# Kernel tuning notes

Hardware: AMD Instinct MI355X
Metric: run time of the kernel (lower is better)

Reference implementation:

```python
import jax, jax.numpy as jnp
import numpy as np

N, E, MUL, NATTR, NBASIS, HID = 50000, 800000, 32, 16, 8, 8
AVG_NEIGH = 16.0


def setup_inputs() -> dict:
    key = jax.random.key(0)
    ks = jax.random.split(key, 13)
    return {
        "x": jax.random.normal(ks[0], (N, NATTR), jnp.float32),
        "h": jax.random.normal(ks[1], (N, 4 * MUL), jnp.float32),
        "edge_length_embeddings": jax.random.uniform(ks[2], (E, NBASIS), jnp.float32),
        "edge_sh": jax.random.normal(ks[3], (E, 4), jnp.float32),
        "edge_index": jax.random.randint(ks[4], (2, E), 0, N),
        "W1_s": jax.random.normal(ks[5], (MUL, MUL), jnp.float32),
        "W1_v": jax.random.normal(ks[6], (MUL, MUL), jnp.float32),
        "fc_w1": jax.random.normal(ks[7], (NBASIS, HID), jnp.float32),
        "fc_w2": jax.random.normal(ks[8], (HID, 4 * MUL), jnp.float32),
        "Wsc_s": jax.random.normal(ks[9], (MUL, NATTR, MUL), jnp.float32),
        "Wsc_v": jax.random.normal(ks[10], (MUL, NATTR, MUL), jnp.float32),
        "W2_s": jax.random.normal(ks[11], (2 * MUL, MUL), jnp.float32),
        "W2_v": jax.random.normal(ks[12], (2 * MUL, MUL), jnp.float32),
    }


def reference(x, h, edge_length_embeddings, edge_sh, edge_index,
              W1_s, W1_v, fc_w1, fc_w2, Wsc_s, Wsc_v, W2_s, W2_v):
    # h layout: [N, 32 scalars (0e) | 32 vectors (1o) flattened]
    h_s0 = h[:, :MUL]                      # [N, 32]
    h_v0 = h[:, MUL:].reshape(-1, MUL, 3)  # [N, 32, 3]

    # self-connection: FullyConnectedTensorProduct(feat, node_attr 16x0e -> feat)
    inv_sc = float(1.0 / np.sqrt(MUL * NATTR))
    sc_s = jnp.einsum('nu,nv,uvw->nw', h_s0, x, Wsc_s) * inv_sc    # [N, 32]
    sc_v = jnp.einsum('num,nv,uvw->nwm', h_v0, x, Wsc_v) * inv_sc  # [N, 32, 3]

    # linear_1 (per-irrep linear, fan-in normalized)
    inv_m = float(1.0 / np.sqrt(MUL))
    h_s = (h_s0 @ W1_s) * inv_m
    h_v = jnp.einsum('num,uw->nwm', h_v0, W1_v) * inv_m

    # radial MLP: [8] -> silu -> [8] -> [tp.weight_numel = 4*32]
    z = jax.nn.silu((edge_length_embeddings @ fc_w1) * float(1.0 / np.sqrt(NBASIS)))
    w = (z @ fc_w2) * float(1.0 / np.sqrt(HID))        # [E, 128]
    wA, wB, wC, wD = jnp.split(w, 4, axis=1)           # each [E, 32]

    src = edge_index[1]
    dst = edge_index[0]
    hs_e = h_s[src]   # [E, 32]  gather
    hv_e = h_v[src]   # [E, 32, 3]
    sh0 = edge_sh[:, 0:1]   # [E, 1]
    sh1 = edge_sh[:, 1:4]   # [E, 3]

    # 4 'uvu' CG paths (edge mul = 1), per-edge weights from radial MLP
    sA = hs_e * sh0 * wA                                            # 0e x 0e -> 0e
    sD = jnp.einsum('eum,em->eu', hv_e, sh1) * wD * float(1.0 / np.sqrt(3.0))  # 1o x 1o -> 0e
    vB = hs_e[:, :, None] * sh1[:, None, :] * wB[:, :, None]        # 0e x 1o -> 1o
    vC = hv_e * sh0[:, :, None] * wC[:, :, None]                    # 1o x 0e -> 1o

    mid_s = jnp.concatenate([sA, sD], axis=1)   # [E, 64]  (sorted irreps_mid, 0e block)
    mid_v = jnp.concatenate([vB, vC], axis=1)   # [E, 64, 3] (1o block)

    # scatter-sum over destination nodes
    agg_s = jax.ops.segment_sum(mid_s, dst, num_segments=N)
    agg_v = jax.ops.segment_sum(mid_v, dst, num_segments=N)
    inv_n = float(1.0 / np.sqrt(AVG_NEIGH))
    agg_s = agg_s * inv_n
    agg_v = agg_v * inv_n

    # linear_2: 64x0e+64x1o -> 32x0e+32x1o
    inv2 = float(1.0 / np.sqrt(2 * MUL))
    out_s = (agg_s @ W2_s) * inv2 + sc_s
    out_v = jnp.einsum('num,uw->nwm', agg_v, W2_v) * inv2 + sc_v

    return jnp.concatenate([out_s, out_v.reshape(-1, 3 * MUL)], axis=1)  # [N, 128]
```

## Files before the change

### kernel.cpp

```cpp
#include <hip/hip_runtime.h>
#include <hip/hip_bf16.h>

#define NN 50000
#define EE 800000
#define SCAN_B 196

typedef unsigned short u16;
typedef unsigned int u32;
typedef float f32x16 __attribute__((ext_vector_type(16)));
typedef short bf16x8_t __attribute__((ext_vector_type(8)));

__device__ __forceinline__ float bfu2f(u16 b) { return __builtin_bit_cast(float, ((u32)b) << 16); }
__device__ __forceinline__ float lo16(u32 d) { return __builtin_bit_cast(float, d << 16); }
__device__ __forceinline__ float hi16(u32 d) { return __builtin_bit_cast(float, d & 0xffff0000u); }
__device__ __forceinline__ u16 f2bfu(float f) {
    u32 u = __builtin_bit_cast(u32, f);
    u32 r = (u + 0x7fffu + ((u >> 16) & 1u)) >> 16;
    return (u16)r;
}
__device__ __forceinline__ u32 cvt_pk_bf16(float lo, float hi) {
    u32 r;
    asm("v_cvt_pk_bf16_f32 %0, %1, %2" : "=v"(r) : "v"(lo), "v"(hi));
    return r;
}

__global__ __launch_bounds__(256) void k_hist(const int* __restrict__ eidx, int* __restrict__ deg) {
    int e = blockIdx.x * 256 + threadIdx.x;
    atomicAdd(&deg[eidx[e]], 1);
}

__global__ __launch_bounds__(256) void k_scan1(const int* __restrict__ deg, int* __restrict__ bsum) {
    __shared__ int red[256];
    const int tid = threadIdx.x;
    int i = blockIdx.x * 256 + tid;
    int v = (i < NN) ? deg[i] : 0;
    red[tid] = v;
    __syncthreads();
    for (int off = 128; off > 0; off >>= 1) {
        if (tid < off) red[tid] += red[tid + off];
        __syncthreads();
    }
    if (tid == 0) bsum[blockIdx.x] = red[0];
}

__global__ __launch_bounds__(256) void k_scan2(
    const int* __restrict__ deg, const int* __restrict__ bsum, int* __restrict__ row_ptr,
    const float* __restrict__ Wscs, const float* __restrict__ Wscv,
    const float* __restrict__ W1s, const float* __restrict__ W1v,
    u16* __restrict__ wscsT, u16* __restrict__ wscvT,
    u16* __restrict__ w1sT, u16* __restrict__ w1vT)
{
    const int b = blockIdx.x;
    const int tid = threadIdx.x;
    if (b >= SCAN_B) {
        int i = (b - SCAN_B) * 256 + tid;
        if (i < 16384) {
            int u = i >> 9, v = (i >> 5) & 15, w = i & 31;
            wscsT[(u * 32 + w) * 16 + v] = f2bfu(Wscs[i]);
            wscvT[(u * 32 + w) * 16 + v] = f2bfu(Wscv[i]);
        }
        if (i < 1024) {
            int u = i >> 5, w = i & 31;
            w1sT[w * 32 + u] = f2bfu(W1s[i]);
            w1vT[w * 32 + u] = f2bfu(W1v[i]);
        }
        return;
    }
    __shared__ int pre[256];
    __shared__ int bpre;
    int pv = (tid < b) ? bsum[tid] : 0;
    pre[tid] = pv;
    __syncthreads();
    for (int off = 128; off > 0; off >>= 1) {
        if (tid < off) pre[tid] += pre[tid + off];
        __syncthreads();
    }
    if (tid == 0) bpre = pre[0];
    __syncthreads();
    int i = b * 256 + tid;
    int v = (i < NN) ? deg[i] : 0;
    pre[tid] = v;
    __syncthreads();
    for (int off = 1; off < 256; off <<= 1) {
        int t = (tid >= off) ? pre[tid - off] : 0;
        __syncthreads();
        pre[tid] += t;
        __syncthreads();
    }
    int excl = pre[tid] - v;
    if (i <= NN) row_ptr[i] = bpre + excl;
}

__global__ __launch_bounds__(256) void k2a_edge(
    const float* __restrict__ emb, const float* __restrict__ esh,
    const int* __restrict__ eidx, const float* __restrict__ fc1,
    const int* __restrict__ row_ptr, int* __restrict__ cursor,
    u32* __restrict__ edata)
{
    __shared__ float sfc1[64];
    const int tid = threadIdx.x;
    if (tid < 64) sfc1[tid] = fc1[tid];
    __syncthreads();
    int e = blockIdx.x * 256 + tid;
    const float invb = 0.3535533905932738f;
    float4 ea = *(const float4*)(emb + (size_t)e * 8);
    float4 eb = *(const float4*)(emb + (size_t)e * 8 + 4);
    float em[8] = {ea.x, ea.y, ea.z, ea.w, eb.x, eb.y, eb.z, eb.w};
    float z[8];
#pragma unroll
    for (int k = 0; k < 8; k++) {
        float t = 0.f;
#pragma unroll
        for (int j = 0; j < 8; j++) t += em[j] * sfc1[j * 8 + k];
        t *= invb;
        z[k] = (t / (1.f + __expf(-t))) * invb;
    }
    float4 sh = *(const float4*)(esh + (size_t)e * 4);
    int dst = eidx[e], src = eidx[EE + e];
    int p = atomicAdd(&cursor[dst], 1);
    size_t slot = (size_t)row_ptr[dst] + p;
    u32* wp = edata + slot * 8;
    uint4 A, B;
    A.x = cvt_pk_bf16(z[0], z[1]);
    A.y = cvt_pk_bf16(z[2], z[3]);
    A.z = cvt_pk_bf16(z[4], z[5]);
    A.w = cvt_pk_bf16(z[6], z[7]);
    B.x = cvt_pk_bf16(sh.x, sh.y);
    B.y = cvt_pk_bf16(sh.z, sh.w);
    B.z = ((u32)src) << 8;
    B.w = 0;
    *(uint4*)wp = A;
    *(uint4*)(wp + 4) = B;
}

__global__ __launch_bounds__(64) void k1_mfma(
    const float* __restrict__ x, const float* __restrict__ h,
    const u16* __restrict__ wscsT, const u16* __restrict__ wscvT,
    const u16* __restrict__ w1sT, const u16* __restrict__ w1vT,
    u16* __restrict__ hsv, float* __restrict__ out)
{
    __shared__ __align__(16) u16 sh[64 * 32 * 2];
    u32* sh32 = (u32*)sh;
    const int l = threadIdx.x;
    const int base = blockIdx.x * 32;
    const int n = l & 31;
    const int hi = l >> 5;

    {
        int r = base + (l >> 1);
        if (r >= NN) r = NN - 1;
        const float* hp = h + (size_t)r * 128 + (l & 1) * 64;
        int nn = l >> 1;
        int cp0 = (l & 1) * 32;
#pragma unroll
        for (int q = 0; q < 16; q++) {
            float4 f = *(const float4*)(hp + q * 4);
            sh32[(cp0 + 2 * q + 0) * 32 + nn] = cvt_pk_bf16(f.x, f.y);
            sh32[(cp0 + 2 * q + 1) * 32 + nn] = cvt_pk_bf16(f.z, f.w);
        }
    }
    float xv0, xv1, xv2, xv3, xv4, xv5, xv6, xv7;
    {
        int r = base + n;
        if (r >= NN) r = NN - 1;
        const float* xp = x + (size_t)r * 16 + hi * 8;
        float4 a = *(const float4*)xp;
        float4 b = *(const float4*)(xp + 4);
        xv0 = a.x; xv1 = a.y; xv2 = a.z; xv3 = a.w;
        xv4 = b.x; xv5 = b.y; xv6 = b.z; xv7 = b.w;
    }
    __syncthreads();

    f32x16 accS, accX, accY, accZ;
#pragma unroll
    for (int i = 0; i < 16; i++) { accS[i] = 0.f; accX[i] = 0.f; accY[i] = 0.f; accZ[i] = 0.f; }

#define MK_A(A, s)                                                     \
    { union { u32 w[4]; bf16x8_t v; } t_;                              \
      t_.w[0] = cvt_pk_bf16((s) * xv0, (s) * xv1);                     \
      t_.w[1] = cvt_pk_bf16((s) * xv2, (s) * xv3);                     \
      t_.w[2] = cvt_pk_bf16((s) * xv4, (s) * xv5);                     \
      t_.w[3] = cvt_pk_bf16((s) * xv6, (s) * xv7);                     \
      A = t_.v; }

    const size_t boff = (size_t)n * 16 + hi * 8;
    bf16x8_t Bs = *(const bf16x8_t*)(wscsT + boff);
    bf16x8_t Bv = *(const bf16x8_t*)(wscvT + boff);
#pragma unroll 2
    for (int u = 0; u < 32; u++) {
        bf16x8_t BsN, BvN;
        if (u < 31) {
            BsN = *(const bf16x8_t*)(wscsT + (size_t)(u + 1) * 512 + boff);
            BvN = *(const bf16x8_t*)(wscvT + (size_t)(u + 1) * 512 + boff);
        }
        float hsu = bfu2f(sh[(u >> 1) * 64 + n * 2 + (u & 1)]);
        int c = 32 + 3 * u;
        float hx = bfu2f(sh[(c >> 1) * 64 + n * 2 + (c & 1)]);
        float hy = bfu2f(sh[((c + 1) >> 1) * 64 + n * 2 + ((c + 1) & 1)]);
        float hz = bfu2f(sh[((c + 2) >> 1) * 64 + n * 2 + ((c + 2) & 1)]);
        bf16x8_t A;
        MK_A(A, hsu); accS = __builtin_amdgcn_mfma_f32_32x32x16_bf16(A, Bs, accS, 0, 0, 0);
        MK_A(A, hx);  accX = __builtin_amdgcn_mfma_f32_32x32x16_bf16(A, Bv, accX, 0, 0, 0);
        MK_A(A, hy);  accY = __builtin_amdgcn_mfma_f32_32x32x16_bf16(A, Bv, accY, 0, 0, 0);
        MK_A(A, hz);  accZ = __builtin_amdgcn_mfma_f32_32x32x16_bf16(A, Bv, accZ, 0, 0, 0);
        Bs = BsN; Bv = BvN;
    }
#undef MK_A

    const float inv_sc = 0.04419417382415922f;
#pragma unroll
    for (int r = 0; r < 16; r++) {
        int node2 = base + ((r & 3) + 8 * (r >> 2) + 4 * hi);
        if (node2 < NN) {
            float* op = out + (size_t)node2 * 128;
            op[n] = accS[r] * inv_sc;
            op[32 + n * 3 + 0] = accX[r] * inv_sc;
            op[32 + n * 3 + 1] = accY[r] * inv_sc;
            op[32 + n * 3 + 2] = accZ[r] * inv_sc;
        }
    }

    const float inv_m = 0.17677669529663687f;
    {
        f32x16 aw;
#pragma unroll
        for (int i = 0; i < 16; i++) aw[i] = 0.f;
#pragma unroll
        for (int k0 = 0; k0 < 2; k0++) {
            union { u32 w[4]; bf16x8_t v; } A;
#pragma unroll
            for (int q = 0; q < 4; q++)
                A.w[q] = sh32[(8 * k0 + 4 * hi + q) * 32 + n];
            bf16x8_t B = *(const bf16x8_t*)(w1sT + n * 32 + 16 * k0 + 8 * hi);
            aw = __builtin_amdgcn_mfma_f32_32x32x16_bf16(A.v, B, aw, 0, 0, 0);
        }
#pragma unroll
        for (int r = 0; r < 16; r++) {
            int node2 = base + ((r & 3) + 8 * (r >> 2) + 4 * hi);
            if (node2 < NN) hsv[(size_t)node2 * 128 + n] = f2bfu(aw[r] * inv_m);
        }
    }
#pragma unroll
    for (int m = 0; m < 3; m++) {
        f32x16 aw;
#pragma unroll
        for (int i = 0; i < 16; i++) aw[i] = 0.f;
#pragma unroll
        for (int k0 = 0; k0 < 2; k0++) {
            union { u32 w[4]; bf16x8_t v; } A;
#pragma unroll
            for (int j = 0; j < 8; j += 2) {
                int u0 = 16 * k0 + 8 * hi + j;
                int c0 = 32 + 3 * u0 + m, c1 = c0 + 3;
                u16 a = sh[(c0 >> 1) * 64 + n * 2 + (c0 & 1)];
                u16 b = sh[(c1 >> 1) * 64 + n * 2 + (c1 & 1)];
                A.w[j >> 1] = (u32)a | ((u32)b << 16);
            }
            bf16x8_t B = *(const bf16x8_t*)(w1vT + n * 32 + 16 * k0 + 8 * hi);
            aw = __builtin_amdgcn_mfma_f32_32x32x16_bf16(A.v, B, aw, 0, 0, 0);
        }
#pragma unroll
        for (int r = 0; r < 16; r++) {
            int node2 = base + ((r & 3) + 8 * (r >> 2) + 4 * hi);
            if (node2 < NN) hsv[(size_t)node2 * 128 + 32 + m * 32 + n] = f2bfu(aw[r] * inv_m);
        }
    }
}

__device__ __forceinline__ void edge_body(
    const u32* __restrict__ r, const char* __restrict__ hbase,
    const float* fcs, const float* fcv, bool lo, int o1, int o2, int o3,
    float& acc_s, float& av0, float& av1, float& av2)
{
    uint4 A = *(const uint4*)r;
    uint4 B = *(const uint4*)(r + 4);
    float ws_ = lo16(A.x) * fcs[0] + hi16(A.x) * fcs[1] + lo16(A.y) * fcs[2] + hi16(A.y) * fcs[3]
              + lo16(A.z) * fcs[4] + hi16(A.z) * fcs[5] + lo16(A.w) * fcs[6] + hi16(A.w) * fcs[7];
    float wv_ = lo16(A.x) * fcv[0] + hi16(A.x) * fcv[1] + lo16(A.y) * fcv[2] + hi16(A.y) * fcv[3]
              + lo16(A.z) * fcv[4] + hi16(A.z) * fcv[5] + lo16(A.w) * fcv[6] + hi16(A.w) * fcv[7];
    float sh0 = lo16(B.x), sx = hi16(B.x), sy = lo16(B.y), sz = hi16(B.y);
    const u16* hp = (const u16*)(hbase + B.z);
    float g1 = bfu2f(hp[o1]), g2 = bfu2f(hp[o2]), g3 = bfu2f(hp[o3]);
    float c1 = lo ? sh0 : sx;
    float c2 = lo ? 0.f : sy;
    float c3 = lo ? 0.f : sz;
    acc_s += ws_ * (g1 * c1 + g2 * c2 + g3 * c3);
    float tw = wv_ * sh0;
    float t0 = lo ? wv_ * sx : tw;
    float t1 = lo ? wv_ * sy : tw;
    float t2 = lo ? wv_ * sz : tw;
    av0 += g1 * t0; av1 += g2 * t1; av2 += g3 * t2;
}

__global__ __launch_bounds__(256) void k2b_gather(
    const u32* __restrict__ edata, const float* __restrict__ fc2,
    const u16* __restrict__ hsv, const int* __restrict__ row_ptr,
    const float* __restrict__ W2s, const float* __restrict__ W2v,
    float* __restrict__ out)
{
    __shared__ float sred[4][256];
    const int tid = threadIdx.x;
    const int wv = tid >> 6, lane = tid & 63;
    const int n = blockIdx.x * 4 + wv;
    const int beg = __builtin_amdgcn_readfirstlane(row_ptr[n]);
    const int end = __builtin_amdgcn_readfirstlane(row_ptr[n + 1]);

    const float inv3 = 0.5773502691896258f;
    const int u = lane & 31;
    const bool lo = lane < 32;
    const int cs = lo ? lane : (96 + u);
    const int cv = lo ? (32 + u) : (64 + u);
    const int o1 = lo ? u : (32 + u);
    const int o2 = lo ? u : (64 + u);
    const int o3 = lo ? u : (96 + u);
    float fcs[8], fcv[8];
#pragma unroll
    for (int j = 0; j < 8; j++) {
        float sscale = lo ? 1.f : inv3;
        fcs[j] = fc2[j * 128 + cs] * sscale;
        fcv[j] = fc2[j * 128 + cv];
    }
    const char* hbase = (const char*)hsv;

    float as[4] = {0.f, 0.f, 0.f, 0.f};
    float a0[4] = {0.f, 0.f, 0.f, 0.f};
    float a1[4] = {0.f, 0.f, 0.f, 0.f};
    float a2[4] = {0.f, 0.f, 0.f, 0.f};
    int s = beg;
    for (; s + 3 < end; s += 4) {
        edge_body(edata + (size_t)(s + 0) * 8, hbase, fcs, fcv, lo, o1, o2, o3, as[0], a0[0], a1[0], a2[0]);
        edge_body(edata + (size_t)(s + 1) * 8, hbase, fcs, fcv, lo, o1, o2, o3, as[1], a0[1], a1[1], a2[1]);
        edge_body(edata + (size_t)(s + 2) * 8, hbase, fcs, fcv, lo, o1, o2, o3, as[2], a0[2], a1[2], a2[2]);
        edge_body(edata + (size_t)(s + 3) * 8, hbase, fcs, fcv, lo, o1, o2, o3, as[3], a0[3], a1[3], a2[3]);
    }
    for (; s < end; s++)
        edge_body(edata + (size_t)s * 8, hbase, fcs, fcv, lo, o1, o2, o3, as[0], a0[0], a1[0], a2[0]);
    float acc_s = (as[0] + as[1]) + (as[2] + as[3]);
    float av0 = (a0[0] + a0[1]) + (a0[2] + a0[3]);
    float av1 = (a1[0] + a1[1]) + (a1[2] + a1[3]);
    float av2 = (a2[0] + a2[1]) + (a2[2] + a2[3]);

    float* red = sred[wv];
    red[lane] = acc_s;
    red[64 + lane * 3 + 0] = av0;
    red[64 + lane * 3 + 1] = av1;
    red[64 + lane * 3 + 2] = av2;

    const float sc2 = 0.03125f;
    const int w = lane & 31;
    const int b0 = lo ? 0 : 64;
    const int s0 = lo ? 1 : 3;
    const int b1 = lo ? 66 : 65;
    const float* __restrict__ Wp0 = lo ? W2s : W2v;
    float p0 = 0.f, p1 = 0.f;
#pragma unroll 8
    for (int c = 0; c < 64; c++) {
        float r0 = red[b0 + c * s0];
        float r1 = red[b1 + c * 3];
        p0 += r0 * Wp0[c * 32 + w];
        p1 += r1 * W2v[c * 32 + w];
    }
    const size_t o = (size_t)n * 128;
    const int addr0 = lo ? w : (32 + 3 * w);
    const int addr1 = lo ? (32 + 3 * w + 2) : (32 + 3 * w + 1);
    out[o + addr0] += p0 * sc2;
    out[o + addr1] += p1 * sc2;
}

extern "C" void kernel_launch(void* const* d_in, const int* in_sizes, int n_in,
                              void* d_out, int out_size, void* d_ws, size_t ws_size,
                              hipStream_t stream) {
    const float* x    = (const float*)d_in[0];
    const float* h    = (const float*)d_in[1];
    const float* emb  = (const float*)d_in[2];
    const float* esh  = (const float*)d_in[3];
    const int*   eidx = (const int*)d_in[4];
    const float* W1s  = (const float*)d_in[5];
    const float* W1v  = (const float*)d_in[6];
    const float* fc1  = (const float*)d_in[7];
    const float* fc2  = (const float*)d_in[8];
    const float* Wscs = (const float*)d_in[9];
    const float* Wscv = (const float*)d_in[10];
    const float* W2s  = (const float*)d_in[11];
    const float* W2v  = (const float*)d_in[12];
    float* out = (float*)d_out;

    int* deg      = (int*)d_ws;
    int* row_ptr  = deg + NN;
    int* cursor   = row_ptr + (NN + 1);
    int* bsum     = (int*)d_ws + 150004;
    u32* edata    = (u32*)d_ws + 150208;
    u16* hsv      = (u16*)(edata + (size_t)EE * 8);
    u16* wscsT    = hsv + (size_t)NN * 128;
    u16* wscvT    = wscsT + 16384;
    u16* w1sT     = wscvT + 16384;
    u16* w1vT     = w1sT + 1024;

    hipMemsetAsync(d_ws, 0, (size_t)(3 * NN + 1) * 4, stream);
    k_hist<<<3125, 256, 0, stream>>>(eidx, deg);
    k_scan1<<<SCAN_B, 256, 0, stream>>>(deg, bsum);
    k_scan2<<<SCAN_B + 64, 256, 0, stream>>>(deg, bsum, row_ptr,
                                             Wscs, Wscv, W1s, W1v, wscsT, wscvT, w1sT, w1vT);
    k2a_edge<<<3125, 256, 0, stream>>>(emb, esh, eidx, fc1, row_ptr, cursor, edata);
    k1_mfma<<<(NN + 31) / 32, 64, 0, stream>>>(x, h, wscsT, wscvT, w1sT, w1vT, hsv, out);
    k2b_gather<<<NN / 4, 256, 0, stream>>>(edata, fc2, hsv, row_ptr, W2s, W2v, out);
}
```

Measured before the change: 238.3 us.

## Interleave hsv node layout and fuse node/edge prep kernels

Stores each node's transformed features interleaved per channel (scalar plus three vector components side by side). The gather kernel can then fetch all four values a lane needs with one 8-byte load instead of three scattered 2-byte loads. Two kernel pairs are merged to cut launches and let independent work overlap: weight conversion now runs inside the histogram kernel, and the per-edge radial/CSR fill shares one launch with the per-node MFMA tiles, four waves per block. In exchange, lanes in the low half of each wave load bytes they do not use, and the combined kernel carries extra shared memory per block.

```diff
diff --git a/kernel.cpp b/kernel.cpp
--- a/kernel.cpp
+++ b/kernel.cpp
@@ -24,9 +24,30 @@
     return r;
 }
 
-__global__ __launch_bounds__(256) void k_hist(const int* __restrict__ eidx, int* __restrict__ deg) {
-    int e = blockIdx.x * 256 + threadIdx.x;
-    atomicAdd(&deg[eidx[e]], 1);
+__global__ __launch_bounds__(256) void k_prep(
+    const int* __restrict__ eidx, int* __restrict__ deg,
+    const float* __restrict__ Wscs, const float* __restrict__ Wscv,
+    const float* __restrict__ W1s, const float* __restrict__ W1v,
+    u16* __restrict__ wscsT, u16* __restrict__ wscvT,
+    u16* __restrict__ w1sT, u16* __restrict__ w1vT)
+{
+    const int b = blockIdx.x;
+    if (b < 3125) {
+        int e = b * 256 + threadIdx.x;
+        atomicAdd(&deg[eidx[e]], 1);
+    } else {
+        int i = (b - 3125) * 256 + threadIdx.x;
+        if (i < 16384) {
+            int u = i >> 9, v = (i >> 5) & 15, w = i & 31;
+            wscsT[(u * 32 + w) * 16 + v] = f2bfu(Wscs[i]);
+            wscvT[(u * 32 + w) * 16 + v] = f2bfu(Wscv[i]);
+        }
+        if (i < 1024) {
+            int u = i >> 5, w = i & 31;
+            w1sT[w * 32 + u] = f2bfu(W1s[i]);
+            w1vT[w * 32 + u] = f2bfu(W1v[i]);
+        }
+    }
 }
 
 __global__ __launch_bounds__(256) void k_scan1(const int* __restrict__ deg, int* __restrict__ bsum) {
@@ -44,28 +65,10 @@
 }
 
 __global__ __launch_bounds__(256) void k_scan2(
-    const int* __restrict__ deg, const int* __restrict__ bsum, int* __restrict__ row_ptr,
-    const float* __restrict__ Wscs, const float* __restrict__ Wscv,
-    const float* __restrict__ W1s, const float* __restrict__ W1v,
-    u16* __restrict__ wscsT, u16* __restrict__ wscvT,
-    u16* __restrict__ w1sT, u16* __restrict__ w1vT)
+    const int* __restrict__ deg, const int* __restrict__ bsum, int* __restrict__ row_ptr)
 {
     const int b = blockIdx.x;
     const int tid = threadIdx.x;
-    if (b >= SCAN_B) {
-        int i = (b - SCAN_B) * 256 + tid;
-        if (i < 16384) {
-            int u = i >> 9, v = (i >> 5) & 15, w = i & 31;
-            wscsT[(u * 32 + w) * 16 + v] = f2bfu(Wscs[i]);
-            wscvT[(u * 32 + w) * 16 + v] = f2bfu(Wscv[i]);
-        }
-        if (i < 1024) {
-            int u = i >> 5, w = i & 31;
-            w1sT[w * 32 + u] = f2bfu(W1s[i]);
-            w1vT[w * 32 + u] = f2bfu(W1v[i]);
-        }
-        return;
-    }
     __shared__ int pre[256];
     __shared__ int bpre;
     int pv = (tid < b) ? bsum[tid] : 0;
@@ -91,58 +94,14 @@
     if (i <= NN) row_ptr[i] = bpre + excl;
 }
 
-__global__ __launch_bounds__(256) void k2a_edge(
-    const float* __restrict__ emb, const float* __restrict__ esh,
-    const int* __restrict__ eidx, const float* __restrict__ fc1,
-    const int* __restrict__ row_ptr, int* __restrict__ cursor,
-    u32* __restrict__ edata)
-{
-    __shared__ float sfc1[64];
-    const int tid = threadIdx.x;
-    if (tid < 64) sfc1[tid] = fc1[tid];
-    __syncthreads();
-    int e = blockIdx.x * 256 + tid;
-    const float invb = 0.3535533905932738f;
-    float4 ea = *(const float4*)(emb + (size_t)e * 8);
-    float4 eb = *(const float4*)(emb + (size_t)e * 8 + 4);
-    float em[8] = {ea.x, ea.y, ea.z, ea.w, eb.x, eb.y, eb.z, eb.w};
-    float z[8];
-#pragma unroll
-    for (int k = 0; k < 8; k++) {
-        float t = 0.f;
-#pragma unroll
-        for (int j = 0; j < 8; j++) t += em[j] * sfc1[j * 8 + k];
-        t *= invb;
-        z[k] = (t / (1.f + __expf(-t))) * invb;
-    }
-    float4 sh = *(const float4*)(esh + (size_t)e * 4);
-    int dst = eidx[e], src = eidx[EE + e];
-    int p = atomicAdd(&cursor[dst], 1);
-    size_t slot = (size_t)row_ptr[dst] + p;
-    u32* wp = edata + slot * 8;
-    uint4 A, B;
-    A.x = cvt_pk_bf16(z[0], z[1]);
-    A.y = cvt_pk_bf16(z[2], z[3]);
-    A.z = cvt_pk_bf16(z[4], z[5]);
-    A.w = cvt_pk_bf16(z[6], z[7]);
-    B.x = cvt_pk_bf16(sh.x, sh.y);
-    B.y = cvt_pk_bf16(sh.z, sh.w);
-    B.z = ((u32)src) << 8;
-    B.w = 0;
-    *(uint4*)wp = A;
-    *(uint4*)(wp + 4) = B;
-}
-
-__global__ __launch_bounds__(64) void k1_mfma(
+__device__ __forceinline__ void k1_tile(
+    int base, int l, u16* __restrict__ sh,
     const float* __restrict__ x, const float* __restrict__ h,
     const u16* __restrict__ wscsT, const u16* __restrict__ wscvT,
     const u16* __restrict__ w1sT, const u16* __restrict__ w1vT,
     u16* __restrict__ hsv, float* __restrict__ out)
 {
-    __shared__ __align__(16) u16 sh[64 * 32 * 2];
     u32* sh32 = (u32*)sh;
-    const int l = threadIdx.x;
-    const int base = blockIdx.x * 32;
     const int n = l & 31;
     const int hi = l >> 5;
 
@@ -237,7 +196,7 @@
 #pragma unroll
         for (int r = 0; r < 16; r++) {
             int node2 = base + ((r & 3) + 8 * (r >> 2) + 4 * hi);
-            if (node2 < NN) hsv[(size_t)node2 * 128 + n] = f2bfu(aw[r] * inv_m);
+            if (node2 < NN) hsv[(size_t)node2 * 128 + n * 4] = f2bfu(aw[r] * inv_m);
         }
     }
 #pragma unroll
@@ -262,14 +221,68 @@
 #pragma unroll
         for (int r = 0; r < 16; r++) {
             int node2 = base + ((r & 3) + 8 * (r >> 2) + 4 * hi);
-            if (node2 < NN) hsv[(size_t)node2 * 128 + 32 + m * 32 + n] = f2bfu(aw[r] * inv_m);
-        }
+            if (node2 < NN) hsv[(size_t)node2 * 128 + n * 4 + 1 + m] = f2bfu(aw[r] * inv_m);
+        }
+    }
+}
+
+__global__ __launch_bounds__(256) void k2a1(
+    const float* __restrict__ emb, const float* __restrict__ esh,
+    const int* __restrict__ eidx, const float* __restrict__ fc1,
+    const int* __restrict__ row_ptr, int* __restrict__ cursor,
+    u32* __restrict__ edata,
+    const float* __restrict__ x, const float* __restrict__ h,
+    const u16* __restrict__ wscsT, const u16* __restrict__ wscvT,
+    const u16* __restrict__ w1sT, const u16* __restrict__ w1vT,
+    u16* __restrict__ hsv, float* __restrict__ out)
+{
+    __shared__ float sfc1[64];
+    __shared__ __align__(16) u16 shh[4][4096];
+    const int b = blockIdx.x;
+    const int tid = threadIdx.x;
+    if (b < 3125) {
+        if (tid < 64) sfc1[tid] = fc1[tid];
+        __syncthreads();
+        int e = b * 256 + tid;
+        const float invb = 0.3535533905932738f;
+        float4 ea = *(const float4*)(emb + (size_t)e * 8);
+        float4 eb = *(const float4*)(emb + (size_t)e * 8 + 4);
+        float em[8] = {ea.x, ea.y, ea.z, ea.w, eb.x, eb.y, eb.z, eb.w};
+        float z[8];
+#pragma unroll
+        for (int k = 0; k < 8; k++) {
+            float t = 0.f;
+#pragma unroll
+            for (int j = 0; j < 8; j++) t += em[j] * sfc1[j * 8 + k];
+            t *= invb;
+            z[k] = (t / (1.f + __expf(-t))) * invb;
+        }
+        float4 sh = *(const float4*)(esh + (size_t)e * 4);
+        int dst = eidx[e], src = eidx[EE + e];
+        int p = atomicAdd(&cursor[dst], 1);
+        size_t slot = (size_t)row_ptr[dst] + p;
+        u32* wp = edata + slot * 8;
+        uint4 A, B;
+        A.x = cvt_pk_bf16(z[0], z[1]);
+        A.y = cvt_pk_bf16(z[2], z[3]);
+        A.z = cvt_pk_bf16(z[4], z[5]);
+        A.w = cvt_pk_bf16(z[6], z[7]);
+        B.x = cvt_pk_bf16(sh.x, sh.y);
+        B.y = cvt_pk_bf16(sh.z, sh.w);
+        B.z = ((u32)src) << 8;
+        B.w = 0;
+        *(uint4*)wp = A;
+        *(uint4*)(wp + 4) = B;
+    } else {
+        const int wv = tid >> 6, l = tid & 63;
+        int tile = (b - 3125) * 4 + wv;
+        k1_tile(tile * 32, l, shh[wv], x, h, wscsT, wscvT, w1sT, w1vT, hsv, out);
     }
 }
 
 __device__ __forceinline__ void edge_body(
-    const u32* __restrict__ r, const char* __restrict__ hbase,
-    const float* fcs, const float* fcv, bool lo, int o1, int o2, int o3,
+    const u32* __restrict__ r, const char* __restrict__ hlane,
+    const float* fcs, const float* fcv, bool lo,
     float& acc_s, float& av0, float& av1, float& av2)
 {
     uint4 A = *(const uint4*)r;
@@ -279,8 +292,11 @@
     float wv_ = lo16(A.x) * fcv[0] + hi16(A.x) * fcv[1] + lo16(A.y) * fcv[2] + hi16(A.y) * fcv[3]
               + lo16(A.z) * fcv[4] + hi16(A.z) * fcv[5] + lo16(A.w) * fcv[6] + hi16(A.w) * fcv[7];
     float sh0 = lo16(B.x), sx = hi16(B.x), sy = lo16(B.y), sz = hi16(B.y);
-    const u16* hp = (const u16*)(hbase + B.z);
-    float g1 = bfu2f(hp[o1]), g2 = bfu2f(hp[o2]), g3 = bfu2f(hp[o3]);
+    uint2 q = *(const uint2*)(hlane + B.z);
+    float ga = lo16(q.x);
+    float g1 = lo ? ga : hi16(q.x);
+    float g2 = lo ? ga : lo16(q.y);
+    float g3 = lo ? ga : hi16(q.y);
     float c1 = lo ? sh0 : sx;
     float c2 = lo ? 0.f : sy;
     float c3 = lo ? 0.f : sz;
@@ -310,9 +326,6 @@
     const bool lo = lane < 32;
     const int cs = lo ? lane : (96 + u);
     const int cv = lo ? (32 + u) : (64 + u);
-    const int o1 = lo ? u : (32 + u);
-    const int o2 = lo ? u : (64 + u);
-    const int o3 = lo ? u : (96 + u);
     float fcs[8], fcv[8];
 #pragma unroll
     for (int j = 0; j < 8; j++) {
@@ -320,7 +333,7 @@
         fcs[j] = fc2[j * 128 + cs] * sscale;
         fcv[j] = fc2[j * 128 + cv];
     }
-    const char* hbase = (const char*)hsv;
+    const char* hlane = (const char*)hsv + u * 8;
 
     float as[4] = {0.f, 0.f, 0.f, 0.f};
     float a0[4] = {0.f, 0.f, 0.f, 0.f};
@@ -328,13 +341,13 @@
     float a2[4] = {0.f, 0.f, 0.f, 0.f};
     int s = beg;
     for (; s + 3 < end; s += 4) {
-        edge_body(edata + (size_t)(s + 0) * 8, hbase, fcs, fcv, lo, o1, o2, o3, as[0], a0[0], a1[0], a2[0]);
-        edge_body(edata + (size_t)(s + 1) * 8, hbase, fcs, fcv, lo, o1, o2, o3, as[1], a0[1], a1[1], a2[1]);
-        edge_body(edata + (size_t)(s + 2) * 8, hbase, fcs, fcv, lo, o1, o2, o3, as[2], a0[2], a1[2], a2[2]);
-        edge_body(edata + (size_t)(s + 3) * 8, hbase, fcs, fcv, lo, o1, o2, o3, as[3], a0[3], a1[3], a2[3]);
+        edge_body(edata + (size_t)(s + 0) * 8, hlane, fcs, fcv, lo, as[0], a0[0], a1[0], a2[0]);
+        edge_body(edata + (size_t)(s + 1) * 8, hlane, fcs, fcv, lo, as[1], a0[1], a1[1], a2[1]);
+        edge_body(edata + (size_t)(s + 2) * 8, hlane, fcs, fcv, lo, as[2], a0[2], a1[2], a2[2]);
+        edge_body(edata + (size_t)(s + 3) * 8, hlane, fcs, fcv, lo, as[3], a0[3], a1[3], a2[3]);
     }
     for (; s < end; s++)
-        edge_body(edata + (size_t)s * 8, hbase, fcs, fcv, lo, o1, o2, o3, as[0], a0[0], a1[0], a2[0]);
+        edge_body(edata + (size_t)s * 8, hlane, fcs, fcv, lo, as[0], a0[0], a1[0], a2[0]);
     float acc_s = (as[0] + as[1]) + (as[2] + as[3]);
     float av0 = (a0[0] + a0[1]) + (a0[2] + a0[3]);
     float av1 = (a1[0] + a1[1]) + (a1[2] + a1[3]);
@@ -397,11 +410,10 @@
     u16* w1vT     = w1sT + 1024;
 
     hipMemsetAsync(d_ws, 0, (size_t)(3 * NN + 1) * 4, stream);
-    k_hist<<<3125, 256, 0, stream>>>(eidx, deg);
+    k_prep<<<3189, 256, 0, stream>>>(eidx, deg, Wscs, Wscv, W1s, W1v, wscsT, wscvT, w1sT, w1vT);
     k_scan1<<<SCAN_B, 256, 0, stream>>>(deg, bsum);
-    k_scan2<<<SCAN_B + 64, 256, 0, stream>>>(deg, bsum, row_ptr,
-                                             Wscs, Wscv, W1s, W1v, wscsT, wscvT, w1sT, w1vT);
-    k2a_edge<<<3125, 256, 0, stream>>>(emb, esh, eidx, fc1, row_ptr, cursor, edata);
-    k1_mfma<<<(NN + 31) / 32, 64, 0, stream>>>(x, h, wscsT, wscvT, w1sT, w1vT, hsv, out);
+    k_scan2<<<SCAN_B, 256, 0, stream>>>(deg, bsum, row_ptr);
+    k2a1<<<3125 + 391, 256, 0, stream>>>(emb, esh, eidx, fc1, row_ptr, cursor, edata,
+                                         x, h, wscsT, wscvT, w1sT, w1vT, hsv, out);
     k2b_gather<<<NN / 4, 256, 0, stream>>>(edata, fc2, hsv, row_ptr, W2s, W2v, out);
 }
```

Measured after the change: 274.9 us. +15.4%, slower.
